# Optimization experiments

Hardware: AMD Instinct MI355X
Metric: run time of the kernel (lower is better)

Reference implementation:

```python
import jax, jax.numpy as jnp
import numpy as np

B, I, A_IN = 32, 32, 16     # batch, input capsules, input atoms
OD, OA = 10, 16             # output_dim (classes), output_atoms
H, W = 12, 12               # spatial grid
NUM_ROUTING = 3


def _squash(t):
    # squash over atom dim (axis=2): x/|x| * |x|^2/(1+|x|^2) = x*|x|/(1+|x|^2)
    norm = jnp.linalg.norm(t, axis=2, keepdims=True)
    return t * norm / (1.0 + norm * norm)


def setup_inputs() -> dict:
    key = jax.random.key(0)
    k1, k2 = jax.random.split(key)
    x = jax.random.normal(k1, (B, I, A_IN, H, W), dtype=jnp.float32)
    # torch weight: (I, A_IN, OD*OA, 1, 1), init N(0, 0.1)
    weight = 0.1 * jax.random.normal(k2, (I, A_IN, OD * OA), dtype=jnp.float32)
    # torch bias: (OD, OA, 1, 1), init const 0.1
    bias = jnp.full((OD, OA, 1, 1), 0.1, dtype=jnp.float32)
    return {"x": x, "weight": weight, "bias": bias}


def reference(x, weight, bias):
    # votes: sum over input atoms -> [B, I, OD*OA, H, W] -> [B, I, OD, OA, H, W]
    votes = jnp.einsum("biahw,iak->bikhw", x, weight)
    votes = votes.reshape(B, I, OD, OA, H, W)
    biases = jnp.broadcast_to(bias, (OD, OA, H, W))

    # Dynamic routing. In the original, logits carry no gradient (built from
    # .data), so intermediate iterations are fully stop-gradient.
    votes_sg = jax.lax.stop_gradient(votes)
    logits = jnp.zeros((B, I, OD, H, W), dtype=votes.dtype)
    activation = None
    for i in range(NUM_ROUTING):
        route = jax.nn.softmax(logits, axis=2)  # softmax over output_dim
        v = votes if i == NUM_ROUTING - 1 else votes_sg
        preact = jnp.einsum("bidhw,bidahw->bdahw", route, v) + biases
        activation = _squash(preact)  # [B, OD, OA, H, W]
        if i < NUM_ROUTING - 1:
            # agreement (dot over atoms) updates logits
            logits = logits + jnp.einsum(
                "bidahw,bdahw->bidhw", votes_sg, jax.lax.stop_gradient(activation)
            )
    return activation
```

## Files before the change

kernel.cpp:

```cpp
#include <hip/hip_runtime.h>
#include <math.h>

#define NB 32
#define NI 32
#define NA 16
#define NOD 10
#define NOA 16
#define NK 160
#define NHW 144
#define NROUT 3
#define NROWS (NB*NHW)
#define VOTES_BYTES ((size_t)NI * NROWS * NK * 2)

__device__ __forceinline__ unsigned short f2bf(float f) {
    unsigned b = __builtin_bit_cast(unsigned, f);
    b += 0x7fffu + ((b >> 16) & 1u);
    return (unsigned short)(b >> 16);
}
__device__ __forceinline__ float bf2f(unsigned short u) {
    return __builtin_bit_cast(float, (unsigned)u << 16);
}
__device__ __forceinline__ float bf_lo(unsigned d) {
    return __builtin_bit_cast(float, d << 16);
}
__device__ __forceinline__ float bf_hi(unsigned d) {
    return __builtin_bit_cast(float, d & 0xffff0000u);
}

__global__ __launch_bounds__(256)
void votes_kernel(const float* __restrict__ x,
                  const float* __restrict__ weight,
                  unsigned short* __restrict__ votes)
{
    __shared__ float sx[72][20];

    const int i   = blockIdx.x >> 6;
    const int b   = (blockIdx.x >> 1) & 31;
    const int hw0 = (blockIdx.x & 1) * 72;
    const int tid = threadIdx.x;

    {
        const float* xb = x + ((size_t)(b * NI + i) * NA) * NHW + hw0;
        for (int j = tid; j < NA * 18; j += 256) {
            const int a  = j / 18;
            const int hq = j % 18;
            const float4 v = *reinterpret_cast<const float4*>(xb + a * NHW + hq * 4);
            sx[hq * 4 + 0][a] = v.x;
            sx[hq * 4 + 1][a] = v.y;
            sx[hq * 4 + 2][a] = v.z;
            sx[hq * 4 + 3][a] = v.w;
        }
    }
    __syncthreads();

    if (tid < 240) {
        const int kq  = tid % 40;
        const int grp = tid / 40;
        const int k0  = kq * 4;
        const int hwb = grp * 12;
        const float4* wp = reinterpret_cast<const float4*>(
            weight + (size_t)i * NA * NK + k0);

        float acc[48];
#pragma unroll
        for (int q = 0; q < 48; ++q) acc[q] = 0.f;

#pragma unroll
        for (int ab = 0; ab < NA; ab += 4) {
            float xr[48];
#pragma unroll
            for (int h = 0; h < 12; ++h) {
                const float4 t = *reinterpret_cast<const float4*>(&sx[hwb + h][ab]);
                xr[h * 4 + 0] = t.x; xr[h * 4 + 1] = t.y;
                xr[h * 4 + 2] = t.z; xr[h * 4 + 3] = t.w;
            }
#pragma unroll
            for (int e = 0; e < 4; ++e) {
                const float4 w4 = wp[(size_t)(ab + e) * 40];
#pragma unroll
                for (int h = 0; h < 12; ++h) {
                    const float xv = xr[h * 4 + e];
                    acc[h * 4 + 0] = fmaf(xv, w4.x, acc[h * 4 + 0]);
                    acc[h * 4 + 1] = fmaf(xv, w4.y, acc[h * 4 + 1]);
                    acc[h * 4 + 2] = fmaf(xv, w4.z, acc[h * 4 + 2]);
                    acc[h * 4 + 3] = fmaf(xv, w4.w, acc[h * 4 + 3]);
                }
            }
        }
        unsigned short* vbase =
            votes + ((size_t)i * NROWS + b * NHW + hw0 + hwb) * NK + k0;
#pragma unroll
        for (int h = 0; h < 12; ++h) {
            const ushort4 s = make_ushort4(f2bf(acc[h * 4 + 0]), f2bf(acc[h * 4 + 1]),
                                           f2bf(acc[h * 4 + 2]), f2bf(acc[h * 4 + 3]));
            *reinterpret_cast<ushort4*>(vbase + (size_t)h * NK) = s;
        }
    }
}

#define P 2
#define SVLD 168

__global__ __launch_bounds__(320)
void routing_kernel(const unsigned short* __restrict__ votes,
                    const float* __restrict__ bias,
                    float* __restrict__ out)
{
    __shared__ unsigned short sv[P * NI * SVLD];
    __shared__ float srt[P][NOD][33];
    __shared__ float sact[P][NOD][NOA];

    const int row0 = blockIdx.x * P;
    const int tid  = threadIdx.x;

    {
        const uint4* src = reinterpret_cast<const uint4*>(votes);
        for (int u = tid; u < NI * P * 20; u += 320) {
            const int i = u / (P * 20);
            const int r = u % (P * 20);
            const int p = r / 20;
            const int c = r % 20;
            *reinterpret_cast<uint4*>(&sv[(p * NI + i) * SVLD + c * 8]) =
                src[(size_t)(i * NROWS + row0 + p) * 20 + c];
        }
    }

    float lg[NOD];
#pragma unroll
    for (int od = 0; od < NOD; ++od) lg[od] = 0.f;
    const int pown = tid >> 5;
    const int iown = tid & 31;
    __syncthreads();

    for (int it = 0; it < NROUT; ++it) {
        if (tid < P * NI) {
            float m = lg[0];
#pragma unroll
            for (int od = 1; od < NOD; ++od) m = fmaxf(m, lg[od]);
            float e[NOD];
            float s = 0.f;
#pragma unroll
            for (int od = 0; od < NOD; ++od) {
                e[od] = __expf(lg[od] - m);
                s += e[od];
            }
            const float inv = 1.f / s;
#pragma unroll
            for (int od = 0; od < NOD; ++od) srt[pown][od][iown] = e[od] * inv;
        }
        __syncthreads();

        if (tid < P * 40) {
            const int p  = tid / 40;
            const int kq = tid % 40;
            const int k0 = kq * 4;
            const int od = kq >> 2;
            const float4 b4 = *reinterpret_cast<const float4*>(bias + k0);
            float a0 = b4.x, a1 = b4.y, a2 = b4.z, a3 = b4.w;
            const unsigned short* svp = &sv[(p * NI) * SVLD + k0];
#pragma unroll
            for (int i = 0; i < NI; ++i) {
                const uint2 d = *reinterpret_cast<const uint2*>(svp + i * SVLD);
                const float r = srt[p][od][i];
                a0 = fmaf(r, bf_lo(d.x), a0);
                a1 = fmaf(r, bf_hi(d.x), a1);
                a2 = fmaf(r, bf_lo(d.y), a2);
                a3 = fmaf(r, bf_hi(d.y), a3);
            }
            float ss = a0 * a0 + a1 * a1 + a2 * a2 + a3 * a3;
            ss += __shfl_xor(ss, 1, 4);
            ss += __shfl_xor(ss, 2, 4);
            const float scale = sqrtf(ss) / (1.f + ss);
            const float4 o = make_float4(a0 * scale, a1 * scale, a2 * scale, a3 * scale);
            *reinterpret_cast<float4*>(&sact[p][od][(kq & 3) * 4]) = o;
        }
        __syncthreads();

        if (it < NROUT - 1) {
            for (int t = tid; t < P * NOD * NI; t += 320) {
                const int p  = t / (NOD * NI);
                const int r  = t % (NOD * NI);
                const int od = r / NI;
                const int i  = r % NI;
                const uint4 d0 = *reinterpret_cast<const uint4*>(
                    &sv[(p * NI + i) * SVLD + od * NOA]);
                const uint4 d1 = *reinterpret_cast<const uint4*>(
                    &sv[(p * NI + i) * SVLD + od * NOA + 8]);
                const float4 c0 = *reinterpret_cast<const float4*>(&sact[p][od][0]);
                const float4 c1 = *reinterpret_cast<const float4*>(&sact[p][od][4]);
                const float4 c2 = *reinterpret_cast<const float4*>(&sact[p][od][8]);
                const float4 c3 = *reinterpret_cast<const float4*>(&sact[p][od][12]);
                float acc;
                acc  = bf_lo(d0.x) * c0.x;
                acc = fmaf(bf_hi(d0.x), c0.y, acc);
                acc = fmaf(bf_lo(d0.y), c0.z, acc);
                acc = fmaf(bf_hi(d0.y), c0.w, acc);
                acc = fmaf(bf_lo(d0.z), c1.x, acc);
                acc = fmaf(bf_hi(d0.z), c1.y, acc);
                acc = fmaf(bf_lo(d0.w), c1.z, acc);
                acc = fmaf(bf_hi(d0.w), c1.w, acc);
                acc = fmaf(bf_lo(d1.x), c2.x, acc);
                acc = fmaf(bf_hi(d1.x), c2.y, acc);
                acc = fmaf(bf_lo(d1.y), c2.z, acc);
                acc = fmaf(bf_hi(d1.y), c2.w, acc);
                acc = fmaf(bf_lo(d1.z), c3.x, acc);
                acc = fmaf(bf_hi(d1.z), c3.y, acc);
                acc = fmaf(bf_lo(d1.w), c3.z, acc);
                acc = fmaf(bf_hi(d1.w), c3.w, acc);
                srt[p][od][i] = acc;
            }
            __syncthreads();
            if (tid < P * NI) {
#pragma unroll
                for (int od = 0; od < NOD; ++od) lg[od] += srt[pown][od][iown];
            }
        }
    }

    if (tid < NK) {
        const int b  = row0 / NHW;
        const int hw = row0 % NHW;
        const int od = tid >> 4;
        const int oa = tid & 15;
        const float2 v = make_float2(sact[0][od][oa], sact[1][od][oa]);
        *reinterpret_cast<float2*>(out + ((size_t)b * NK + tid) * NHW + hw) = v;
    }
}

#define FP 2
#define FSVLD 168

__global__ __launch_bounds__(512)
void capsule_fallback_kernel(const float* __restrict__ x,
                             const float* __restrict__ weight,
                             const float* __restrict__ bias,
                             float* __restrict__ out)
{
    __shared__ float sx[NI][NA][FP];
    __shared__ unsigned short svf[FP * NI * FSVLD];
    __shared__ float slog[FP][NI][NOD];
    __shared__ float srtf[FP][NI][NOD];
    __shared__ float sactf[FP][NOD][NOA];

    const int bk  = blockIdx.x;
    const int b   = bk / (NHW / FP);
    const int hw0 = (bk % (NHW / FP)) * FP;
    const int tid = threadIdx.x;
#define FSVIDX(p, i, k) (((p) * NI + (i)) * FSVLD + (k))

    if (tid < NI * NA) {
        const int i = tid >> 4;
        const int a = tid & (NA - 1);
        const float2 v = *reinterpret_cast<const float2*>(
            x + (size_t)((b * NI + i) * NA + a) * NHW + hw0);
        sx[i][a][0] = v.x;
        sx[i][a][1] = v.y;
    }
    {
        float* lf = &slog[0][0][0];
        for (int j = tid; j < FP * NI * NOD; j += 512) lf[j] = 0.0f;
    }
    __syncthreads();

    for (int j = tid; j < NI * (NK / 4); j += 512) {
        const int i  = j / (NK / 4);
        const int k0 = (j - i * (NK / 4)) * 4;
        const float4* wp = reinterpret_cast<const float4*>(weight + (size_t)i * NA * NK + k0);
        float4 a0 = make_float4(0.f, 0.f, 0.f, 0.f);
        float4 a1 = make_float4(0.f, 0.f, 0.f, 0.f);
#pragma unroll
        for (int a = 0; a < NA; ++a) {
            const float4 w4 = wp[a * (NK / 4)];
            const float2 xa = *reinterpret_cast<const float2*>(&sx[i][a][0]);
            a0.x = fmaf(xa.x, w4.x, a0.x); a0.y = fmaf(xa.x, w4.y, a0.y);
            a0.z = fmaf(xa.x, w4.z, a0.z); a0.w = fmaf(xa.x, w4.w, a0.w);
            a1.x = fmaf(xa.y, w4.x, a1.x); a1.y = fmaf(xa.y, w4.y, a1.y);
            a1.z = fmaf(xa.y, w4.z, a1.z); a1.w = fmaf(xa.y, w4.w, a1.w);
        }
        ushort4 s0 = make_ushort4(f2bf(a0.x), f2bf(a0.y), f2bf(a0.z), f2bf(a0.w));
        ushort4 s1 = make_ushort4(f2bf(a1.x), f2bf(a1.y), f2bf(a1.z), f2bf(a1.w));
        *reinterpret_cast<ushort4*>(&svf[FSVIDX(0, i, k0)]) = s0;
        *reinterpret_cast<ushort4*>(&svf[FSVIDX(1, i, k0)]) = s1;
    }
    __syncthreads();

    for (int it = 0; it < NROUT; ++it) {
        if (tid < FP * NI) {
            const int p = tid >> 5;
            const int i = tid & 31;
            float m = slog[p][i][0];
#pragma unroll
            for (int od = 1; od < NOD; ++od) m = fmaxf(m, slog[p][i][od]);
            float e[NOD];
            float s = 0.0f;
#pragma unroll
            for (int od = 0; od < NOD; ++od) {
                e[od] = __expf(slog[p][i][od] - m);
                s += e[od];
            }
            const float inv = 1.0f / s;
#pragma unroll
            for (int od = 0; od < NOD; ++od) srtf[p][i][od] = e[od] * inv;
        }
        __syncthreads();

        if (tid < FP * NK) {
            const int p  = tid / NK;
            const int k  = tid - p * NK;
            const int od = k >> 4;
            const int oa = k & (NOA - 1);
            float acc = bias[k];
            const unsigned short* svp = &svf[FSVIDX(p, 0, k)];
#pragma unroll
            for (int i = 0; i < NI; ++i)
                acc = fmaf(srtf[p][i][od], bf2f(svp[i * FSVLD]), acc);
            float ss = acc * acc;
#pragma unroll
            for (int m = 1; m < NOA; m <<= 1)
                ss += __shfl_xor(ss, m, NOA);
            const float scale = sqrtf(ss) / (1.0f + ss);
            sactf[p][od][oa] = acc * scale;
        }
        __syncthreads();

        if (it < NROUT - 1) {
            for (int j = tid; j < FP * NI * NOD; j += 512) {
                const int p  = j / (NI * NOD);
                const int r  = j - p * (NI * NOD);
                const int od = r >> 5;
                const int i  = r & 31;
                const uint4 d0 = *reinterpret_cast<const uint4*>(&svf[FSVIDX(p, i, od * NOA)]);
                const uint4 d1 = *reinterpret_cast<const uint4*>(&svf[FSVIDX(p, i, od * NOA + 8)]);
                const float* ap = &sactf[p][od][0];
                float acc;
                acc  = bf_lo(d0.x) * ap[0];
                acc = fmaf(bf_hi(d0.x), ap[1], acc);
                acc = fmaf(bf_lo(d0.y), ap[2], acc);
                acc = fmaf(bf_hi(d0.y), ap[3], acc);
                acc = fmaf(bf_lo(d0.z), ap[4], acc);
                acc = fmaf(bf_hi(d0.z), ap[5], acc);
                acc = fmaf(bf_lo(d0.w), ap[6], acc);
                acc = fmaf(bf_hi(d0.w), ap[7], acc);
                acc = fmaf(bf_lo(d1.x), ap[8], acc);
                acc = fmaf(bf_hi(d1.x), ap[9], acc);
                acc = fmaf(bf_lo(d1.y), ap[10], acc);
                acc = fmaf(bf_hi(d1.y), ap[11], acc);
                acc = fmaf(bf_lo(d1.z), ap[12], acc);
                acc = fmaf(bf_hi(d1.z), ap[13], acc);
                acc = fmaf(bf_lo(d1.w), ap[14], acc);
                acc = fmaf(bf_hi(d1.w), ap[15], acc);
                slog[p][i][od] += acc;
            }
            __syncthreads();
        }
    }

    __syncthreads();
    if (tid < NK) {
        const int od = tid >> 4;
        const int oa = tid & (NOA - 1);
        const float2 v = make_float2(sactf[0][od][oa], sactf[1][od][oa]);
        *reinterpret_cast<float2*>(out + (size_t)(b * NK + tid) * NHW + hw0) = v;
    }
}

extern "C" void kernel_launch(void* const* d_in, const int* in_sizes, int n_in,
                              void* d_out, int out_size, void* d_ws, size_t ws_size,
                              hipStream_t stream) {
    const float* x      = (const float*)d_in[0];
    const float* weight = (const float*)d_in[1];
    const float* bias   = (const float*)d_in[2];
    float* out          = (float*)d_out;

    if (ws_size >= VOTES_BYTES) {
        unsigned short* votes = (unsigned short*)d_ws;
        votes_kernel<<<NI * NB * 2, 256, 0, stream>>>(x, weight, votes);
        routing_kernel<<<NROWS / P, 320, 0, stream>>>(votes, bias, out);
    } else {
        capsule_fallback_kernel<<<NB * (NHW / FP), 512, 0, stream>>>(x, weight, bias, out);
    }
}
```

Baseline: 54.13 us.

## Assign one wavefront per spatial row in routing kernel, using wave barriers

Restructures the routing kernel so each 64-lane wavefront owns one (batch, hw) row. Block-wide __syncthreads between routing phases become intra-wave barriers, and each block now covers four rows. Work is remapped to 2 atoms per lane for the preact sum, and the output becomes a float4 store over four consecutive hw positions. This is meant to remove block-level synchronisation and idle threads, at the cost of more shared memory per block and a less balanced tail (lanes below 16 handle the last two classes).

```diff
diff --git a/kernel.cpp b/kernel.cpp
--- a/kernel.cpp
+++ b/kernel.cpp
@@ -98,42 +98,47 @@
     }
 }
 
-#define P 2
 #define SVLD 168
 
-__global__ __launch_bounds__(320)
+__global__ __launch_bounds__(256)
 void routing_kernel(const unsigned short* __restrict__ votes,
                     const float* __restrict__ bias,
                     float* __restrict__ out)
 {
-    __shared__ unsigned short sv[P * NI * SVLD];
-    __shared__ float srt[P][NOD][33];
-    __shared__ float sact[P][NOD][NOA];
-
-    const int row0 = blockIdx.x * P;
-    const int tid  = threadIdx.x;
+    __shared__ unsigned short sv[4][NI][SVLD];
+    __shared__ float srt[4][NOD][33];
+    __shared__ float sact[4][164];
+
+    const int tid = threadIdx.x;
+    const int w   = tid >> 6;
+    const int l   = tid & 63;
+    const int row = blockIdx.x * 4 + w;
 
     {
         const uint4* src = reinterpret_cast<const uint4*>(votes);
-        for (int u = tid; u < NI * P * 20; u += 320) {
-            const int i = u / (P * 20);
-            const int r = u % (P * 20);
-            const int p = r / 20;
-            const int c = r % 20;
-            *reinterpret_cast<uint4*>(&sv[(p * NI + i) * SVLD + c * 8]) =
-                src[(size_t)(i * NROWS + row0 + p) * 20 + c];
-        }
-    }
+#pragma unroll
+        for (int r = 0; r < 10; ++r) {
+            const int idx = l + 64 * r;
+            const int i   = idx / 20;
+            const int c   = idx % 20;
+            *reinterpret_cast<uint4*>(&sv[w][i][c * 8]) =
+                src[((size_t)i * NROWS + row) * 20 + c];
+        }
+    }
+
+    const float2 b0 = *reinterpret_cast<const float2*>(bias + 2 * l);
+    float2 b1 = make_float2(0.f, 0.f);
+    if (l < 16) b1 = *reinterpret_cast<const float2*>(bias + 128 + 2 * l);
 
     float lg[NOD];
 #pragma unroll
     for (int od = 0; od < NOD; ++od) lg[od] = 0.f;
-    const int pown = tid >> 5;
-    const int iown = tid & 31;
-    __syncthreads();
+    const int iown = l & 31;
+
+    __builtin_amdgcn_wave_barrier();
 
     for (int it = 0; it < NROUT; ++it) {
-        if (tid < P * NI) {
+        {
             float m = lg[0];
 #pragma unroll
             for (int od = 1; od < NOD; ++od) m = fmaxf(m, lg[od]);
@@ -145,51 +150,63 @@
                 s += e[od];
             }
             const float inv = 1.f / s;
-#pragma unroll
-            for (int od = 0; od < NOD; ++od) srt[pown][od][iown] = e[od] * inv;
-        }
-        __syncthreads();
-
-        if (tid < P * 40) {
-            const int p  = tid / 40;
-            const int kq = tid % 40;
-            const int k0 = kq * 4;
-            const int od = kq >> 2;
-            const float4 b4 = *reinterpret_cast<const float4*>(bias + k0);
-            float a0 = b4.x, a1 = b4.y, a2 = b4.z, a3 = b4.w;
-            const unsigned short* svp = &sv[(p * NI) * SVLD + k0];
+            if (l < 32) {
+#pragma unroll
+                for (int od = 0; od < NOD; ++od) srt[w][od][iown] = e[od] * inv;
+            }
+        }
+        __builtin_amdgcn_wave_barrier();
+
+        {
+            const int od0 = l >> 3;
+            float a0 = b0.x, a1 = b0.y;
 #pragma unroll
             for (int i = 0; i < NI; ++i) {
-                const uint2 d = *reinterpret_cast<const uint2*>(svp + i * SVLD);
-                const float r = srt[p][od][i];
-                a0 = fmaf(r, bf_lo(d.x), a0);
-                a1 = fmaf(r, bf_hi(d.x), a1);
-                a2 = fmaf(r, bf_lo(d.y), a2);
-                a3 = fmaf(r, bf_hi(d.y), a3);
-            }
-            float ss = a0 * a0 + a1 * a1 + a2 * a2 + a3 * a3;
-            ss += __shfl_xor(ss, 1, 4);
-            ss += __shfl_xor(ss, 2, 4);
-            const float scale = sqrtf(ss) / (1.f + ss);
-            const float4 o = make_float4(a0 * scale, a1 * scale, a2 * scale, a3 * scale);
-            *reinterpret_cast<float4*>(&sact[p][od][(kq & 3) * 4]) = o;
-        }
-        __syncthreads();
+                const unsigned d = *reinterpret_cast<const unsigned*>(&sv[w][i][2 * l]);
+                const float r = srt[w][od0][i];
+                a0 = fmaf(r, bf_lo(d), a0);
+                a1 = fmaf(r, bf_hi(d), a1);
+            }
+            float ss = a0 * a0 + a1 * a1;
+            ss += __shfl_xor(ss, 1, 8);
+            ss += __shfl_xor(ss, 2, 8);
+            ss += __shfl_xor(ss, 4, 8);
+            const float sc = sqrtf(ss) / (1.f + ss);
+            *reinterpret_cast<float2*>(&sact[w][2 * l]) = make_float2(a0 * sc, a1 * sc);
+
+            if (l < 16) {
+                const int od1 = 8 + (l >> 3);
+                float c0 = b1.x, c1 = b1.y;
+#pragma unroll
+                for (int i = 0; i < NI; ++i) {
+                    const unsigned d = *reinterpret_cast<const unsigned*>(&sv[w][i][128 + 2 * l]);
+                    const float r = srt[w][od1][i];
+                    c0 = fmaf(r, bf_lo(d), c0);
+                    c1 = fmaf(r, bf_hi(d), c1);
+                }
+                float s2 = c0 * c0 + c1 * c1;
+                s2 += __shfl_xor(s2, 1, 8);
+                s2 += __shfl_xor(s2, 2, 8);
+                s2 += __shfl_xor(s2, 4, 8);
+                const float sc2 = sqrtf(s2) / (1.f + s2);
+                *reinterpret_cast<float2*>(&sact[w][128 + 2 * l]) =
+                    make_float2(c0 * sc2, c1 * sc2);
+            }
+        }
+        __builtin_amdgcn_wave_barrier();
 
         if (it < NROUT - 1) {
-            for (int t = tid; t < P * NOD * NI; t += 320) {
-                const int p  = t / (NOD * NI);
-                const int r  = t % (NOD * NI);
-                const int od = r / NI;
-                const int i  = r % NI;
-                const uint4 d0 = *reinterpret_cast<const uint4*>(
-                    &sv[(p * NI + i) * SVLD + od * NOA]);
-                const uint4 d1 = *reinterpret_cast<const uint4*>(
-                    &sv[(p * NI + i) * SVLD + od * NOA + 8]);
-                const float4 c0 = *reinterpret_cast<const float4*>(&sact[p][od][0]);
-                const float4 c1 = *reinterpret_cast<const float4*>(&sact[p][od][4]);
-                const float4 c2 = *reinterpret_cast<const float4*>(&sact[p][od][8]);
-                const float4 c3 = *reinterpret_cast<const float4*>(&sact[p][od][12]);
+#pragma unroll
+            for (int r = 0; r < 5; ++r) {
+                const int t  = l + 64 * r;
+                const int i  = t & 31;
+                const int od = t >> 5;
+                const uint4 d0 = *reinterpret_cast<const uint4*>(&sv[w][i][od * NOA]);
+                const uint4 d1 = *reinterpret_cast<const uint4*>(&sv[w][i][od * NOA + 8]);
+                const float4 c0 = *reinterpret_cast<const float4*>(&sact[w][od * NOA + 0]);
+                const float4 c1 = *reinterpret_cast<const float4*>(&sact[w][od * NOA + 4]);
+                const float4 c2 = *reinterpret_cast<const float4*>(&sact[w][od * NOA + 8]);
+                const float4 c3 = *reinterpret_cast<const float4*>(&sact[w][od * NOA + 12]);
                 float acc;
                 acc  = bf_lo(d0.x) * c0.x;
                 acc = fmaf(bf_hi(d0.x), c0.y, acc);
@@ -207,23 +224,23 @@
                 acc = fmaf(bf_hi(d1.z), c3.y, acc);
                 acc = fmaf(bf_lo(d1.w), c3.z, acc);
                 acc = fmaf(bf_hi(d1.w), c3.w, acc);
-                srt[p][od][i] = acc;
-            }
-            __syncthreads();
-            if (tid < P * NI) {
-#pragma unroll
-                for (int od = 0; od < NOD; ++od) lg[od] += srt[pown][od][iown];
-            }
-        }
-    }
-
+                srt[w][od][i] = acc;
+            }
+            __builtin_amdgcn_wave_barrier();
+#pragma unroll
+            for (int od = 0; od < NOD; ++od) lg[od] += srt[w][od][iown];
+            __builtin_amdgcn_wave_barrier();
+        }
+    }
+
+    __syncthreads();
     if (tid < NK) {
-        const int b  = row0 / NHW;
-        const int hw = row0 % NHW;
-        const int od = tid >> 4;
-        const int oa = tid & 15;
-        const float2 v = make_float2(sact[0][od][oa], sact[1][od][oa]);
-        *reinterpret_cast<float2*>(out + ((size_t)b * NK + tid) * NHW + hw) = v;
+        const int b  = row / NHW - (w ? (row / NHW) - (blockIdx.x * 4) / NHW : 0);
+        const int bb = (blockIdx.x * 4) / NHW;
+        const int hw = (blockIdx.x * 4) % NHW;
+        const float4 v = make_float4(sact[0][tid], sact[1][tid],
+                                     sact[2][tid], sact[3][tid]);
+        *reinterpret_cast<float4*>(out + ((size_t)bb * NK + tid) * NHW + hw) = v;
     }
 }
 
@@ -375,7 +392,7 @@
     if (ws_size >= VOTES_BYTES) {
         unsigned short* votes = (unsigned short*)d_ws;
         votes_kernel<<<NI * NB * 2, 256, 0, stream>>>(x, weight, votes);
-        routing_kernel<<<NROWS / P, 320, 0, stream>>>(votes, bias, out);
+        routing_kernel<<<NROWS / 4, 256, 0, stream>>>(votes, bias, out);
     } else {
         capsule_fallback_kernel<<<NB * (NHW / FP), 512, 0, stream>>>(x, weight, bias, out);
     }
```

Result: faster. 44.43 us (-17.9%).
